# Performance work log

Measured on AMD Instinct MI355X. Metric: run time of the kernel, lower is better.

Reference implementation:

```python
import jax, jax.numpy as jnp
import numpy as np

D_MODEL = 1024
NUM_HEADS = 16
D_K = D_MODEL // NUM_HEADS
NEG = jnp.float32(-1e9)  # finite stand-in for -inf to keep softmax NaN-free on fully masked rows


def setup_inputs() -> dict:
    key = jax.random.key(0)
    ks = jax.random.split(key, 7)
    B, N_q, N_kv = 2, 2048, 2048
    x = jax.random.normal(ks[0], (B, N_q, D_MODEL), dtype=jnp.float32)
    K = jax.random.normal(ks[1], (B, NUM_HEADS, N_kv, D_K), dtype=jnp.float32)
    V = jax.random.normal(ks[2], (B, NUM_HEADS, N_kv, D_K), dtype=jnp.float32)
    # pad masks: True = keep. Ensure first kv position is always valid.
    kv_pad_mask = jax.random.uniform(ks[3], (B, 1, 1, N_kv)) > 0.1
    kv_pad_mask = kv_pad_mask.at[..., 0].set(True)
    q_pad_mask = jax.random.uniform(ks[4], (B, 1, N_q, 1)) > 0.1
    # params (torch Linear, bias=False); stored as [in, out] so y = x @ W
    Wq = jax.random.normal(ks[5], (D_MODEL, D_MODEL), dtype=jnp.float32) / np.sqrt(D_MODEL)
    Wo = jax.random.normal(ks[6], (D_MODEL, D_MODEL), dtype=jnp.float32) / np.sqrt(D_MODEL)
    return {"x": x, "K": K, "V": V, "Wq": Wq, "Wo": Wo,
            "kv_pad_mask": kv_pad_mask, "q_pad_mask": q_pad_mask}


def reference(x, K, V, Wq, Wo, kv_pad_mask, q_pad_mask):
    B, N_q, D = x.shape
    H, d_k = NUM_HEADS, D_K
    # Q projection and split into heads: [B, H, N_q, d_k]
    Q = (x @ Wq).reshape(B, N_q, H, d_k).transpose(0, 2, 1, 3)
    scores = jnp.einsum('bhqd,bhkd->bhqk', Q, K) / np.sqrt(d_k).astype(np.float32)
    keep = q_pad_mask & kv_pad_mask  # broadcast to [B,1,N_q,N_kv]
    scores = jnp.where(keep, scores, NEG)
    probs = jax.nn.softmax(scores, axis=-1)
    attn = jnp.einsum('bhqk,bhkd->bhqd', probs, V)  # [B,H,N_q,d_k]
    attn = attn.transpose(0, 2, 1, 3).reshape(B, N_q, H * d_k)
    return attn @ Wo
```

## Files before the change

kernel.cpp:

```cpp
#include <hip/hip_runtime.h>
#include <hip/hip_bf16.h>
#include <stdint.h>

typedef __hip_bfloat16 bf16;
typedef __attribute__((ext_vector_type(8))) short short8;
typedef __attribute__((ext_vector_type(4))) short s16x4;
typedef __attribute__((ext_vector_type(4))) float floatx4;

#define MFMA16(a, b, c) __builtin_amdgcn_mfma_f32_16x16x32_bf16(a, b, c, 0, 0, 0)

__device__ __forceinline__ void async_lds16(const void* g, void* l) {
  __builtin_amdgcn_global_load_lds((__attribute__((address_space(1))) const void*)g,
                                   (__attribute__((address_space(3))) void*)l, 16, 0, 0);
}

__device__ __forceinline__ unsigned rne2(float a, float b) {
  unsigned ua = __float_as_uint(a), ub = __float_as_uint(b);
  ua = ua + 0x7FFFu + ((ua >> 16) & 1u);
  ub = ub + 0x7FFFu + ((ub >> 16) & 1u);
  return (ua >> 16) | (ub & 0xFFFF0000u);
}

__global__ void prep_masks_k(const int* __restrict__ kv, const int* __restrict__ q,
                             float* __restrict__ kvB, float* __restrict__ qB) {
  int i = blockIdx.x * 256 + threadIdx.x;
  kvB[i] = kv[i] ? 0.0f : -3000.0f;
  qB[i]  = q[i]  ? 0.0f : -3000.0f;
}

__global__ void cvt2_k(const float* __restrict__ a, bf16* __restrict__ da,
                       const float* __restrict__ b, bf16* __restrict__ db) {
  int gid = blockIdx.x;
  const float* s; bf16* d;
  if (gid < 4096) { s = a; d = da; } else { s = b; d = db; gid -= 4096; }
  int i = (gid * 256 + threadIdx.x) * 4;
  float4 v = *(const float4*)(s + i);
  uint2 o = {rne2(v.x, v.y), rne2(v.z, v.w)};
  *(uint2*)(d + i) = o;
}

__global__ __launch_bounds__(256) void cvt_transpose_k(const float* __restrict__ src,
                                                       bf16* __restrict__ dst, int R, int C) {
  __shared__ float tile[64][65];
  int m = blockIdx.z;
  int r0 = blockIdx.x * 64, c0 = blockIdx.y * 64;
  const float* s = src + (size_t)m * R * C;
  bf16* d = dst + (size_t)m * R * C;
  int t = threadIdx.x;
  int tr = t >> 2, tg = t & 3;
#pragma unroll
  for (int k = 0; k < 4; ++k) {
    int col = tg * 16 + k * 4;
    float4 v = *(const float4*)(s + (size_t)(r0 + tr) * C + c0 + col);
    tile[tr][col] = v.x; tile[tr][col + 1] = v.y; tile[tr][col + 2] = v.z; tile[tr][col + 3] = v.w;
  }
  __syncthreads();
#pragma unroll
  for (int k = 0; k < 4; ++k) {
    int rr = tg * 16 + k * 4;
    unsigned lo = rne2(tile[rr][tr], tile[rr + 1][tr]);
    unsigned hi = rne2(tile[rr + 2][tr], tile[rr + 3][tr]);
    uint2 o = {lo, hi};
    *(uint2*)(d + (size_t)(c0 + tr) * R + r0 + rr) = o;
  }
}

__global__ __launch_bounds__(256) void cvtT_w_k(const float* __restrict__ w0, bf16* __restrict__ d0,
                                                const float* __restrict__ w1, bf16* __restrict__ d1) {
  __shared__ float tile[64][65];
  const float* s = blockIdx.z ? w1 : w0;
  bf16* d = blockIdx.z ? d1 : d0;
  int r0 = blockIdx.x * 64, c0 = blockIdx.y * 64;
  int t = threadIdx.x;
  int tr = t >> 2, tg = t & 3;
#pragma unroll
  for (int k = 0; k < 4; ++k) {
    int col = tg * 16 + k * 4;
    float4 v = *(const float4*)(s + (size_t)(r0 + tr) * 1024 + c0 + col);
    tile[tr][col] = v.x; tile[tr][col + 1] = v.y; tile[tr][col + 2] = v.z; tile[tr][col + 3] = v.w;
  }
  __syncthreads();
#pragma unroll
  for (int k = 0; k < 4; ++k) {
    int rr = tg * 16 + k * 4;
    uint2 o = {rne2(tile[rr][tr], tile[rr + 1][tr]), rne2(tile[rr + 2][tr], tile[rr + 3][tr])};
    *(uint2*)(d + (size_t)(c0 + tr) * 1024 + r0 + rr) = o;
  }
}

__device__ __forceinline__ void storeC(bf16* C, size_t i, float v) { C[i] = __float2bfloat16(v); }
__device__ __forceinline__ void storeC(float* C, size_t i, float v) { C[i] = v; }

template <typename OT>
__global__ __launch_bounds__(256) void gemm_bt_k(const bf16* __restrict__ A,
                                                 const bf16* __restrict__ BT,
                                                 OT* __restrict__ C,
                                                 int M, int N, int K, float scale) {
  __shared__ __align__(16) bf16 As[128 * 32];
  __shared__ __align__(16) bf16 Bs[64 * 32];
  int tid = threadIdx.x;
  int wave = tid >> 6, lane = tid & 63;
  int quad = lane >> 4, lm = lane & 15;
  int wm = wave >> 1, wn = wave & 1;
  int row0 = blockIdx.y * 128, col0 = blockIdx.x * 64;

  floatx4 acc[4][2];
#pragma unroll
  for (int mt = 0; mt < 4; ++mt)
#pragma unroll
    for (int nt = 0; nt < 2; ++nt) acc[mt][nt] = (floatx4){0.f, 0.f, 0.f, 0.f};

  for (int k0 = 0; k0 < K; k0 += 32) {
    __syncthreads();
#pragma unroll
    for (int ch = 0; ch < 2; ++ch) {
      int e = (wave * 2 + ch) * 512 + lane * 8;
      async_lds16(A + (size_t)(row0 + (e >> 5)) * K + k0 + (e & 31), &As[(wave * 2 + ch) * 512]);
    }
    {
      int e = wave * 512 + lane * 8;
      async_lds16(BT + (size_t)(col0 + (e >> 5)) * K + k0 + (e & 31), &Bs[wave * 512]);
    }
    __syncthreads();
    short8 af[4], bfr[2];
#pragma unroll
    for (int mt = 0; mt < 4; ++mt)
      af[mt] = *(const short8*)&As[(wm * 64 + mt * 16 + lm) * 32 + quad * 8];
#pragma unroll
    for (int nt = 0; nt < 2; ++nt)
      bfr[nt] = *(const short8*)&Bs[(wn * 32 + nt * 16 + lm) * 32 + quad * 8];
#pragma unroll
    for (int mt = 0; mt < 4; ++mt)
#pragma unroll
      for (int nt = 0; nt < 2; ++nt)
        acc[mt][nt] = MFMA16(af[mt], bfr[nt], acc[mt][nt]);
  }
#pragma unroll
  for (int mt = 0; mt < 4; ++mt)
#pragma unroll
    for (int nt = 0; nt < 2; ++nt)
#pragma unroll
      for (int j = 0; j < 4; ++j) {
        int rr = row0 + wm * 64 + mt * 16 + quad * 4 + j;
        int cc = col0 + wn * 32 + nt * 16 + lm;
        storeC(C, (size_t)rr * N + cc, acc[mt][nt][j] * scale);
      }
}

__global__ __launch_bounds__(256, 4) void attn_k(const bf16* __restrict__ Q,
                                                 const bf16* __restrict__ Km,
                                                 const bf16* __restrict__ VT,
                                                 const float* __restrict__ qB,
                                                 const float* __restrict__ kvB,
                                                 float* __restrict__ Opart,
                                                 float* __restrict__ lpart) {
  const float TINY = 9.313225746154785e-10f;
  __shared__ __align__(16) bf16 Ks[64 * 64];
  __shared__ __align__(16) bf16 Vs[64 * 64];
  __shared__ __align__(16) float kvBs[1024];

  int tid = threadIdx.x;
  int wave = tid >> 6, lane = tid & 63;
  int quad = lane >> 4, lm = lane & 15;
  int qb = blockIdx.x & 15, slice = blockIdx.x >> 4;
  int h = blockIdx.y, b = blockIdx.z;
  int q0 = qb * 128 + wave * 32;
  int kvbeg = slice * 1024;

  const bf16* kbase = Km + (size_t)(b * 16 + h) * 2048 * 64;
  const bf16* vbase = VT + (size_t)(b * 16 + h) * 64 * 2048;
  const float* kvBb = kvB + b * 2048;

  async_lds16(kvBb + kvbeg + wave * 256 + lane * 4, &kvBs[wave * 256]);

  short8 aq[2][2];
  float qbias[2];
#pragma unroll
  for (int g = 0; g < 2; ++g) {
    const bf16* qp = Q + (size_t)(b * 2048 + q0 + g * 16 + lm) * 1024 + h * 64 + quad * 8;
    aq[g][0] = *(const short8*)qp;
    aq[g][1] = *(const short8*)(qp + 32);
    qbias[g] = qB[b * 2048 + q0 + g * 16 + lm];
  }

  short8 ones;
#pragma unroll
  for (int i = 0; i < 8; ++i) ones[i] = (short)0x3F80;

  floatx4 o_acc[2][4];
  floatx4 l_acc[2];
#pragma unroll
  for (int g = 0; g < 2; ++g) {
    l_acc[g] = (floatx4){0.f, 0.f, 0.f, 0.f};
#pragma unroll
    for (int t = 0; t < 4; ++t) o_acc[g][t] = (floatx4){0.f, 0.f, 0.f, 0.f};
  }

  union S8U { short8 s8; s16x4 h[2]; unsigned u[4]; };

  for (int kv0 = kvbeg; kv0 < kvbeg + 1024; kv0 += 64) {
    __syncthreads();
#pragma unroll
    for (int c = 0; c < 2; ++c) {
      int o = (wave * 2 + c) * 1024 + lane * 16;
      int r = o >> 7;
      int g16 = (o >> 4) & 7;
      int sc = ((g16 ^ (r & 7)) * 8);
      async_lds16(kbase + (size_t)(kv0 + r) * 64 + sc, &Ks[(wave * 2 + c) * 512]);
      async_lds16(vbase + (size_t)r * 2048 + kv0 + sc, &Vs[(wave * 2 + c) * 512]);
    }
    __syncthreads();

    floatx4 kb4[4];
#pragma unroll
    for (int t = 0; t < 4; ++t)
      kb4[t] = *(const floatx4*)&kvBs[(kv0 - kvbeg) + t * 16 + quad * 4];

    S8U pf[2][2];
#pragma unroll
    for (int t = 0; t < 4; ++t) {
      int R = t * 16 + lm, sw = R & 7;
      short8 kf0 = *(const short8*)&Ks[R * 64 + ((quad ^ sw) * 8)];
      short8 kf1 = *(const short8*)&Ks[R * 64 + (((quad + 4) ^ sw) * 8)];
#pragma unroll
      for (int g = 0; g < 2; ++g) {
        floatx4 z;
#pragma unroll
        for (int j = 0; j < 4; ++j) z[j] = kb4[t][j] + qbias[g];
        z = MFMA16(kf0, aq[g][0], z);
        z = MFMA16(kf1, aq[g][1], z);
        float p0 = __builtin_amdgcn_exp2f(z[0]) + TINY;
        float p1 = __builtin_amdgcn_exp2f(z[1]) + TINY;
        float p2 = __builtin_amdgcn_exp2f(z[2]) + TINY;
        float p3 = __builtin_amdgcn_exp2f(z[3]) + TINY;
        pf[g][t >> 1].u[(t & 1) * 2 + 0] = rne2(p0, p1);
        pf[g][t >> 1].u[(t & 1) * 2 + 1] = rne2(p2, p3);
      }
    }
#pragma unroll
    for (int t = 0; t < 4; ++t) {
      int D = t * 16 + lm, sw = D & 7;
      int hoff = (quad & 1) * 4, qh = quad >> 1;
      S8U vf0, vf1;
      vf0.h[0] = *(const s16x4*)&Vs[D * 64 + (((0 + qh) ^ sw) * 8) + hoff];
      vf0.h[1] = *(const s16x4*)&Vs[D * 64 + (((2 + qh) ^ sw) * 8) + hoff];
      vf1.h[0] = *(const s16x4*)&Vs[D * 64 + (((4 + qh) ^ sw) * 8) + hoff];
      vf1.h[1] = *(const s16x4*)&Vs[D * 64 + (((6 + qh) ^ sw) * 8) + hoff];
#pragma unroll
      for (int g = 0; g < 2; ++g) {
        o_acc[g][t] = MFMA16(vf0.s8, pf[g][0].s8, o_acc[g][t]);
        o_acc[g][t] = MFMA16(vf1.s8, pf[g][1].s8, o_acc[g][t]);
      }
    }
#pragma unroll
    for (int g = 0; g < 2; ++g) {
      l_acc[g] = MFMA16(ones, pf[g][0].s8, l_acc[g]);
      l_acc[g] = MFMA16(ones, pf[g][1].s8, l_acc[g]);
    }
  }
  float* Op = Opart + (size_t)slice * (2u * 2048u * 1024u);
#pragma unroll
  for (int g = 0; g < 2; ++g) {
    int q = b * 2048 + q0 + g * 16 + lm;
#pragma unroll
    for (int t = 0; t < 4; ++t)
      *(floatx4*)(Op + (size_t)q * 1024 + h * 64 + t * 16 + quad * 4) = o_acc[g][t];
    if (quad == 0)
      lpart[((size_t)slice * 2 * 2048 + (size_t)q) * 16 + h] = l_acc[g][0];
  }
}

__global__ void combine_k(const float* __restrict__ Opart, const float* __restrict__ lpart,
                          bf16* __restrict__ out) {
  int i = (blockIdx.x * 256 + threadIdx.x) * 4;
  int bq = i >> 10, h = (i >> 6) & 15;
  float4 a = *(const float4*)(Opart + i);
  float4 c = *(const float4*)(Opart + 4194304 + i);
  float l = lpart[bq * 16 + h] + lpart[65536 + bq * 16 + h];
  float rl = 1.0f / l;
  uint2 o = {rne2((a.x + c.x) * rl, (a.y + c.y) * rl),
             rne2((a.z + c.z) * rl, (a.w + c.w) * rl)};
  *(uint2*)(out + i) = o;
}

extern "C" void kernel_launch(void* const* d_in, const int* in_sizes, int n_in,
                              void* d_out, int out_size, void* d_ws, size_t ws_size,
                              hipStream_t stream) {
  const float* x  = (const float*)d_in[0];
  const float* K  = (const float*)d_in[1];
  const float* V  = (const float*)d_in[2];
  const float* Wq = (const float*)d_in[3];
  const float* Wo = (const float*)d_in[4];
  const int* kvm  = (const int*)d_in[5];
  const int* qm   = (const int*)d_in[6];

  char* w = (char*)d_ws;
  bf16* xb    = (bf16*)(w);
  bf16* attnb = xb;
  bf16* Qb    = (bf16*)(w + (8u << 20));
  bf16* Kb    = (bf16*)(w + (16u << 20));
  bf16* VTb   = (bf16*)(w + (24u << 20));
  bf16* WqT   = (bf16*)(w + (32u << 20));
  bf16* WoT   = (bf16*)(w + (34u << 20));
  float* qB   = (float*)(w + (36u << 20));
  float* kvB  = (float*)(w + (36u << 20) + 16384);
  float* Opart = (float*)(w + (40u << 20));
  float* lpart = (float*)(w + (72u << 20));

  const float SCL2 = 0.18033688011112042f;

  prep_masks_k<<<16, 256, 0, stream>>>(kvm, qm, kvB, qB);
  cvt2_k<<<8192, 256, 0, stream>>>(x, xb, K, Kb);
  cvtT_w_k<<<dim3(16, 16, 2), 256, 0, stream>>>(Wq, WqT, Wo, WoT);
  cvt_transpose_k<<<dim3(32, 1, 32), 256, 0, stream>>>(V, VTb, 2048, 64);

  gemm_bt_k<bf16><<<dim3(16, 32), 256, 0, stream>>>(xb, WqT, Qb, 4096, 1024, 1024, SCL2);
  attn_k<<<dim3(32, 16, 2), 256, 0, stream>>>(Qb, Kb, VTb, qB, kvB, Opart, lpart);
  combine_k<<<4096, 256, 0, stream>>>(Opart, lpart, attnb);
  gemm_bt_k<float><<<dim3(16, 32), 256, 0, stream>>>(attnb, WoT, (float*)d_out, 4096, 1024, 1024, 1.0f);
}
```

Measured before the change: 220.6 us.

## Split attention KV into four slices, store bf16 partials, deepen GEMM K-tile

The attention kernel now splits the KV range into four 512-wide slices instead of two, doubling the grid and raising the occupancy hint to 8 blocks per CU. Partial outputs are stored as bf16 instead of fp32, and the combine kernel sums four slices with 8-wide vector loads. The GEMM stages 64-wide K tiles per sync instead of 32, halving barrier count, and the transpose kernels write 16-byte vectors. The bf16 partials add rounding error before normalization, and the bigger LDS tiles may reduce GEMM occupancy.

```diff
diff --git a/kernel.cpp b/kernel.cpp
--- a/kernel.cpp
+++ b/kernel.cpp
@@ -55,20 +55,25 @@
     tile[tr][col] = v.x; tile[tr][col + 1] = v.y; tile[tr][col + 2] = v.z; tile[tr][col + 3] = v.w;
   }
   __syncthreads();
-#pragma unroll
-  for (int k = 0; k < 4; ++k) {
-    int rr = tg * 16 + k * 4;
-    unsigned lo = rne2(tile[rr][tr], tile[rr + 1][tr]);
-    unsigned hi = rne2(tile[rr + 2][tr], tile[rr + 3][tr]);
-    uint2 o = {lo, hi};
-    *(uint2*)(d + (size_t)(c0 + tr) * R + r0 + rr) = o;
-  }
-}
-
-__global__ __launch_bounds__(256) void cvtT_w_k(const float* __restrict__ w0, bf16* __restrict__ d0,
-                                                const float* __restrict__ w1, bf16* __restrict__ d1) {
+  int orow = t >> 2, ch = t & 3;
+  bf16* drow = d + (size_t)(c0 + orow) * R + r0;
+  uint4 w0, w1;
+  w0.x = rne2(tile[ch * 8 + 0][orow], tile[ch * 8 + 1][orow]);
+  w0.y = rne2(tile[ch * 8 + 2][orow], tile[ch * 8 + 3][orow]);
+  w0.z = rne2(tile[ch * 8 + 4][orow], tile[ch * 8 + 5][orow]);
+  w0.w = rne2(tile[ch * 8 + 6][orow], tile[ch * 8 + 7][orow]);
+  w1.x = rne2(tile[32 + ch * 8 + 0][orow], tile[32 + ch * 8 + 1][orow]);
+  w1.y = rne2(tile[32 + ch * 8 + 2][orow], tile[32 + ch * 8 + 3][orow]);
+  w1.z = rne2(tile[32 + ch * 8 + 4][orow], tile[32 + ch * 8 + 5][orow]);
+  w1.w = rne2(tile[32 + ch * 8 + 6][orow], tile[32 + ch * 8 + 7][orow]);
+  *(uint4*)(drow + ch * 8) = w0;
+  *(uint4*)(drow + 32 + ch * 8) = w1;
+}
+
+__global__ __launch_bounds__(256) void cvtT_w_k(const float* __restrict__ w0p, bf16* __restrict__ d0,
+                                                const float* __restrict__ w1p, bf16* __restrict__ d1) {
   __shared__ float tile[64][65];
-  const float* s = blockIdx.z ? w1 : w0;
+  const float* s = blockIdx.z ? w1p : w0p;
   bf16* d = blockIdx.z ? d1 : d0;
   int r0 = blockIdx.x * 64, c0 = blockIdx.y * 64;
   int t = threadIdx.x;
@@ -80,12 +85,19 @@
     tile[tr][col] = v.x; tile[tr][col + 1] = v.y; tile[tr][col + 2] = v.z; tile[tr][col + 3] = v.w;
   }
   __syncthreads();
-#pragma unroll
-  for (int k = 0; k < 4; ++k) {
-    int rr = tg * 16 + k * 4;
-    uint2 o = {rne2(tile[rr][tr], tile[rr + 1][tr]), rne2(tile[rr + 2][tr], tile[rr + 3][tr])};
-    *(uint2*)(d + (size_t)(c0 + tr) * 1024 + r0 + rr) = o;
-  }
+  int orow = t >> 2, ch = t & 3;
+  bf16* drow = d + (size_t)(c0 + orow) * 1024 + r0;
+  uint4 a, b;
+  a.x = rne2(tile[ch * 8 + 0][orow], tile[ch * 8 + 1][orow]);
+  a.y = rne2(tile[ch * 8 + 2][orow], tile[ch * 8 + 3][orow]);
+  a.z = rne2(tile[ch * 8 + 4][orow], tile[ch * 8 + 5][orow]);
+  a.w = rne2(tile[ch * 8 + 6][orow], tile[ch * 8 + 7][orow]);
+  b.x = rne2(tile[32 + ch * 8 + 0][orow], tile[32 + ch * 8 + 1][orow]);
+  b.y = rne2(tile[32 + ch * 8 + 2][orow], tile[32 + ch * 8 + 3][orow]);
+  b.z = rne2(tile[32 + ch * 8 + 4][orow], tile[32 + ch * 8 + 5][orow]);
+  b.w = rne2(tile[32 + ch * 8 + 6][orow], tile[32 + ch * 8 + 7][orow]);
+  *(uint4*)(drow + ch * 8) = a;
+  *(uint4*)(drow + 32 + ch * 8) = b;
 }
 
 __device__ __forceinline__ void storeC(bf16* C, size_t i, float v) { C[i] = __float2bfloat16(v); }
@@ -96,8 +108,8 @@
                                                  const bf16* __restrict__ BT,
                                                  OT* __restrict__ C,
                                                  int M, int N, int K, float scale) {
-  __shared__ __align__(16) bf16 As[128 * 32];
-  __shared__ __align__(16) bf16 Bs[64 * 32];
+  __shared__ __align__(16) bf16 As[128 * 64];
+  __shared__ __align__(16) bf16 Bs[64 * 64];
   int tid = threadIdx.x;
   int wave = tid >> 6, lane = tid & 63;
   int quad = lane >> 4, lm = lane & 15;
@@ -110,30 +122,34 @@
 #pragma unroll
     for (int nt = 0; nt < 2; ++nt) acc[mt][nt] = (floatx4){0.f, 0.f, 0.f, 0.f};
 
-  for (int k0 = 0; k0 < K; k0 += 32) {
+  for (int k0 = 0; k0 < K; k0 += 64) {
     __syncthreads();
+#pragma unroll
+    for (int ch = 0; ch < 4; ++ch) {
+      int e = (wave * 4 + ch) * 512 + lane * 8;
+      async_lds16(A + (size_t)(row0 + (e >> 6)) * K + k0 + (e & 63), &As[(wave * 4 + ch) * 512]);
+    }
 #pragma unroll
     for (int ch = 0; ch < 2; ++ch) {
       int e = (wave * 2 + ch) * 512 + lane * 8;
-      async_lds16(A + (size_t)(row0 + (e >> 5)) * K + k0 + (e & 31), &As[(wave * 2 + ch) * 512]);
-    }
-    {
-      int e = wave * 512 + lane * 8;
-      async_lds16(BT + (size_t)(col0 + (e >> 5)) * K + k0 + (e & 31), &Bs[wave * 512]);
+      async_lds16(BT + (size_t)(col0 + (e >> 6)) * K + k0 + (e & 63), &Bs[(wave * 2 + ch) * 512]);
     }
     __syncthreads();
-    short8 af[4], bfr[2];
-#pragma unroll
-    for (int mt = 0; mt < 4; ++mt)
-      af[mt] = *(const short8*)&As[(wm * 64 + mt * 16 + lm) * 32 + quad * 8];
-#pragma unroll
-    for (int nt = 0; nt < 2; ++nt)
-      bfr[nt] = *(const short8*)&Bs[(wn * 32 + nt * 16 + lm) * 32 + quad * 8];
-#pragma unroll
-    for (int mt = 0; mt < 4; ++mt)
+#pragma unroll
+    for (int ks = 0; ks < 64; ks += 32) {
+      short8 af[4], bfr[2];
+#pragma unroll
+      for (int mt = 0; mt < 4; ++mt)
+        af[mt] = *(const short8*)&As[(wm * 64 + mt * 16 + lm) * 64 + ks + quad * 8];
 #pragma unroll
       for (int nt = 0; nt < 2; ++nt)
-        acc[mt][nt] = MFMA16(af[mt], bfr[nt], acc[mt][nt]);
+        bfr[nt] = *(const short8*)&Bs[(wn * 32 + nt * 16 + lm) * 64 + ks + quad * 8];
+#pragma unroll
+      for (int mt = 0; mt < 4; ++mt)
+#pragma unroll
+        for (int nt = 0; nt < 2; ++nt)
+          acc[mt][nt] = MFMA16(af[mt], bfr[nt], acc[mt][nt]);
+    }
   }
 #pragma unroll
   for (int mt = 0; mt < 4; ++mt)
@@ -147,17 +163,17 @@
       }
 }
 
-__global__ __launch_bounds__(256, 4) void attn_k(const bf16* __restrict__ Q,
+__global__ __launch_bounds__(256, 8) void attn_k(const bf16* __restrict__ Q,
                                                  const bf16* __restrict__ Km,
                                                  const bf16* __restrict__ VT,
                                                  const float* __restrict__ qB,
                                                  const float* __restrict__ kvB,
-                                                 float* __restrict__ Opart,
+                                                 bf16* __restrict__ Opart,
                                                  float* __restrict__ lpart) {
   const float TINY = 9.313225746154785e-10f;
   __shared__ __align__(16) bf16 Ks[64 * 64];
   __shared__ __align__(16) bf16 Vs[64 * 64];
-  __shared__ __align__(16) float kvBs[1024];
+  __shared__ __align__(16) float kvBs[512];
 
   int tid = threadIdx.x;
   int wave = tid >> 6, lane = tid & 63;
@@ -165,13 +181,14 @@
   int qb = blockIdx.x & 15, slice = blockIdx.x >> 4;
   int h = blockIdx.y, b = blockIdx.z;
   int q0 = qb * 128 + wave * 32;
-  int kvbeg = slice * 1024;
+  int kvbeg = slice * 512;
 
   const bf16* kbase = Km + (size_t)(b * 16 + h) * 2048 * 64;
   const bf16* vbase = VT + (size_t)(b * 16 + h) * 64 * 2048;
   const float* kvBb = kvB + b * 2048;
 
-  async_lds16(kvBb + kvbeg + wave * 256 + lane * 4, &kvBs[wave * 256]);
+  if (wave < 2)
+    async_lds16(kvBb + kvbeg + wave * 256 + lane * 4, &kvBs[wave * 256]);
 
   short8 aq[2][2];
   float qbias[2];
@@ -198,7 +215,7 @@
 
   union S8U { short8 s8; s16x4 h[2]; unsigned u[4]; };
 
-  for (int kv0 = kvbeg; kv0 < kvbeg + 1024; kv0 += 64) {
+  for (int kv0 = kvbeg; kv0 < kvbeg + 512; kv0 += 64) {
     __syncthreads();
 #pragma unroll
     for (int c = 0; c < 2; ++c) {
@@ -258,29 +275,43 @@
       l_acc[g] = MFMA16(ones, pf[g][1].s8, l_acc[g]);
     }
   }
-  float* Op = Opart + (size_t)slice * (2u * 2048u * 1024u);
+  bf16* Op = Opart + (size_t)slice * (2u * 2048u * 1024u);
 #pragma unroll
   for (int g = 0; g < 2; ++g) {
     int q = b * 2048 + q0 + g * 16 + lm;
-#pragma unroll
-    for (int t = 0; t < 4; ++t)
-      *(floatx4*)(Op + (size_t)q * 1024 + h * 64 + t * 16 + quad * 4) = o_acc[g][t];
+    bf16* orow = Op + (size_t)q * 1024 + h * 64;
+#pragma unroll
+    for (int t = 0; t < 4; ++t) {
+      uint2 ov = {rne2(o_acc[g][t][0], o_acc[g][t][1]),
+                  rne2(o_acc[g][t][2], o_acc[g][t][3])};
+      *(uint2*)(orow + t * 16 + quad * 4) = ov;
+    }
     if (quad == 0)
-      lpart[((size_t)slice * 2 * 2048 + (size_t)q) * 16 + h] = l_acc[g][0];
-  }
-}
-
-__global__ void combine_k(const float* __restrict__ Opart, const float* __restrict__ lpart,
+      lpart[((size_t)slice * 4096 + (size_t)q) * 16 + h] = l_acc[g][0];
+  }
+}
+
+__global__ void combine_k(const bf16* __restrict__ Opart, const float* __restrict__ lpart,
                           bf16* __restrict__ out) {
-  int i = (blockIdx.x * 256 + threadIdx.x) * 4;
+  int i = (blockIdx.x * 256 + threadIdx.x) * 8;
   int bq = i >> 10, h = (i >> 6) & 15;
-  float4 a = *(const float4*)(Opart + i);
-  float4 c = *(const float4*)(Opart + 4194304 + i);
-  float l = lpart[bq * 16 + h] + lpart[65536 + bq * 16 + h];
+  float l = lpart[bq * 16 + h] + lpart[65536 + bq * 16 + h] +
+            lpart[131072 + bq * 16 + h] + lpart[196608 + bq * 16 + h];
   float rl = 1.0f / l;
-  uint2 o = {rne2((a.x + c.x) * rl, (a.y + c.y) * rl),
-             rne2((a.z + c.z) * rl, (a.w + c.w) * rl)};
-  *(uint2*)(out + i) = o;
+  float acc[8];
+#pragma unroll
+  for (int e = 0; e < 8; ++e) acc[e] = 0.f;
+#pragma unroll
+  for (int s = 0; s < 4; ++s) {
+    uint4 u = *(const uint4*)(Opart + s * 4194304 + i);
+    acc[0] += __uint_as_float(u.x << 16); acc[1] += __uint_as_float(u.x & 0xFFFF0000u);
+    acc[2] += __uint_as_float(u.y << 16); acc[3] += __uint_as_float(u.y & 0xFFFF0000u);
+    acc[4] += __uint_as_float(u.z << 16); acc[5] += __uint_as_float(u.z & 0xFFFF0000u);
+    acc[6] += __uint_as_float(u.w << 16); acc[7] += __uint_as_float(u.w & 0xFFFF0000u);
+  }
+  uint4 o = {rne2(acc[0] * rl, acc[1] * rl), rne2(acc[2] * rl, acc[3] * rl),
+             rne2(acc[4] * rl, acc[5] * rl), rne2(acc[6] * rl, acc[7] * rl)};
+  *(uint4*)(out + i) = o;
 }
 
 extern "C" void kernel_launch(void* const* d_in, const int* in_sizes, int n_in,
@@ -304,7 +335,7 @@
   bf16* WoT   = (bf16*)(w + (34u << 20));
   float* qB   = (float*)(w + (36u << 20));
   float* kvB  = (float*)(w + (36u << 20) + 16384);
-  float* Opart = (float*)(w + (40u << 20));
+  bf16* Opart = (bf16*)(w + (40u << 20));
   float* lpart = (float*)(w + (72u << 20));
 
   const float SCL2 = 0.18033688011112042f;
@@ -315,7 +346,7 @@
   cvt_transpose_k<<<dim3(32, 1, 32), 256, 0, stream>>>(V, VTb, 2048, 64);
 
   gemm_bt_k<bf16><<<dim3(16, 32), 256, 0, stream>>>(xb, WqT, Qb, 4096, 1024, 1024, SCL2);
-  attn_k<<<dim3(32, 16, 2), 256, 0, stream>>>(Qb, Kb, VTb, qB, kvB, Opart, lpart);
-  combine_k<<<4096, 256, 0, stream>>>(Opart, lpart, attnb);
+  attn_k<<<dim3(64, 16, 2), 256, 0, stream>>>(Qb, Kb, VTb, qB, kvB, Opart, lpart);
+  combine_k<<<2048, 256, 0, stream>>>(Opart, lpart, attnb);
   gemm_bt_k<float><<<dim3(16, 32), 256, 0, stream>>>(attnb, WoT, (float*)d_out, 4096, 1024, 1024, 1.0f);
 }
```

New measurement: 538.1 us. +144.0%, slower.
